# Kernel tuning notes

Measured on AMD Instinct MI355X. Metric: run time of the kernel, lower is better.

Reference implementation:

```python
import jax, jax.numpy as jnp
import numpy as np

TEMPERATURE = 0.1
KNN = 5
NEG = -1e30   # finite stand-in for -inf: identical softmax/threshold result, NaN-safe
EPS = -1e-08  # note: the original code really adds a NEGATIVE epsilon
MASK_VAL = -1.0


def setup_inputs() -> dict:
    key = jax.random.key(0)
    k1, k2, k3, k4 = jax.random.split(key, 4)
    n_img, max_r, n_cap, max_w, d = 128, 36, 128, 32, 512
    imgs = jax.random.normal(k1, (n_img, max_r, d), dtype=jnp.float32)
    caps = jax.random.normal(k2, (n_cap, max_w, d), dtype=jnp.float32)
    img_lens = jax.random.randint(k3, (n_img,), KNN + 1, max_r + 1, dtype=jnp.int32)
    cap_lens = jax.random.randint(k4, (n_cap,), 4, max_w + 1, dtype=jnp.int32)
    # guarantee lens.max() equals the static dims (torch slices to lens.max())
    img_lens = img_lens.at[0].set(max_r)
    cap_lens = cap_lens.at[0].set(max_w)
    return {"imgs": imgs, "caps": caps, "img_lens": img_lens, "cap_lens": cap_lens}


def reference(imgs, caps, img_lens, cap_lens):
    n_img, max_r, d = imgs.shape
    n_cap, max_w, _ = caps.shape
    knn = min(KNN, max_r)

    img_valid = jnp.arange(max_r)[None, :] < img_lens[:, None]   # [n_img, max_r]
    cap_valid = jnp.arange(max_w)[None, :] < cap_lens[:, None]   # [n_cap, max_w]
    imgs = jnp.where(img_valid[..., None], imgs, 0.0)
    caps = jnp.where(cap_valid[..., None], caps, 0.0)

    # fine-grained all-pairs similarities: [n_cap, n_img, max_w, max_r]
    sims = jnp.einsum('cwd,ird->ciwr', caps, imgs) / TEMPERATURE
    mask = cap_valid[:, None, :, None] & img_valid[None, :, None, :]
    sims = jnp.where(mask, sims, NEG)

    # top-KNN threshold along region axis (== sort()[..., max_r-KNN] in torch)
    kth = jax.lax.top_k(sims, knn)[0][..., -1:]
    sims = jnp.where(sims < kth, NEG, sims)

    attn = jax.nn.softmax(sims, axis=-1)
    attn = jnp.where(mask, attn, 0.0)

    att = jnp.einsum('ciwr,ird->ciwd', attn, imgs)                # attended regions
    num = jnp.einsum('ciwd,cwd->ciw', att, caps)
    den = jnp.linalg.norm(att, axis=-1) + EPS
    out = num / den                                               # [n_cap, n_img, max_w]
    out = jnp.where(cap_valid[:, None, :], out, MASK_VAL)
    return jnp.transpose(out, (1, 0, 2))                          # [n_img, n_cap, max_w]
```

## Files before the change

### kernel.cpp

```cpp
#include <hip/hip_runtime.h>
#include <cmath>

#define N_IMG 128
#define MAX_R 36
#define N_CAP 128
#define MAX_W 32
#define DIM   512
#define NEGV  -1e30f

typedef unsigned short u16;
typedef unsigned int   u32;
typedef unsigned char  u8;
typedef __attribute__((ext_vector_type(4))) int i32x4;

#define NI_ELEMS (N_IMG * MAX_R * DIM)
#define NC_ELEMS (N_CAP * MAX_W * DIM)

#define A_CHUNK 18432
#define B_CHUNK 16384
#define BUF_BYTES 34816
#define LDS_BYTES 69632

__device__ __forceinline__ void gload_lds16(const void* g, void* l) {
    __builtin_amdgcn_global_load_lds(
        (const __attribute__((address_space(1))) void*)g,
        (__attribute__((address_space(3))) void*)l, 16, 0, 0);
}

__global__ __launch_bounds__(256) void convert_kernel(const float* __restrict__ imgs,
                                                      const float* __restrict__ caps,
                                                      u8* __restrict__ imgsT,
                                                      u8* __restrict__ capsT) {
    const size_t ni4 = NI_ELEMS / 4;
    const size_t total4 = (NI_ELEMS + NC_ELEMS) / 4;
    const size_t stride = (size_t)gridDim.x * blockDim.x;
    for (size_t p = (size_t)blockIdx.x * blockDim.x + threadIdx.x; p < total4; p += stride) {
        const bool isImg = p < ni4;
        const float4 v = isImg ? ((const float4*)imgs)[p] : ((const float4*)caps)[p - ni4];
        const int q0 = (int)rintf(fminf(fmaxf(v.x * 4096.f, -32639.f), 32639.f));
        const int q1 = (int)rintf(fminf(fmaxf(v.y * 4096.f, -32639.f), 32639.f));
        const int q2 = (int)rintf(fminf(fmaxf(v.z * 4096.f, -32639.f), 32639.f));
        const int q3 = (int)rintf(fminf(fmaxf(v.w * 4096.f, -32639.f), 32639.f));
        const int h0 = (q0 + 128) >> 8, l0 = q0 - (h0 << 8);
        const int h1 = (q1 + 128) >> 8, l1 = q1 - (h1 << 8);
        const int h2 = (q2 + 128) >> 8, l2 = q2 - (h2 << 8);
        const int h3 = (q3 + 128) >> 8, l3 = q3 - (h3 << 8);
        const u32 hw = (u32)(h0 & 255) | ((u32)(h1 & 255) << 8) |
                       ((u32)(h2 & 255) << 16) | ((u32)(h3 & 255) << 24);
        const u32 lw = (u32)(l0 & 255) | ((u32)(l1 & 255) << 8) |
                       ((u32)(l2 & 255) << 16) | ((u32)(l3 & 255) << 24);
        if (isImg) {
            const int e = (int)(p * 4);
            const int imgRow = e >> 9, k = e & 511;
            const int g = imgRow / 144;
            const int rowT = imgRow - g * 144;
            const int kb = k >> 6, k6 = k & 63;
            const int blk = (k6 >> 4) ^ ((rowT >> 1) & 3);
            const size_t off = (size_t)(g * 8 + kb) * A_CHUNK + rowT * 64 + blk * 16 + (k6 & 15);
            *(u32*)(imgsT + off) = hw;
            *(u32*)(imgsT + off + 9216) = lw;
        } else {
            const int e = (int)((p - ni4) * 4);
            const int R = e >> 9, k = e & 511;
            const int cg = R >> 7, row = R & 127;
            const int kb = k >> 6, k6 = k & 63;
            const int blk = (k6 >> 4) ^ ((row >> 1) & 3);
            const size_t off = (size_t)(cg * 8 + kb) * B_CHUNK + row * 64 + blk * 16 + (k6 & 15);
            *(u32*)(capsT + off) = hw;
            *(u32*)(capsT + off + 8192) = lw;
        }
    }
}

__global__ __launch_bounds__(256) void gram_i8_kernel(const u8* __restrict__ imgsT,
                                                      float* __restrict__ G) {
    const int i  = blockIdx.x;
    const int gg = i >> 2;
    const int m  = i & 3;
    const int t = threadIdx.x;
    const int wid = t >> 6;
    const int lane = t & 63;
    const int l15 = lane & 15;
    const int kq = lane >> 4;

    __shared__ __align__(16) u8 sT[2][2][3072];

    const u8* base = imgsT + (size_t)gg * 8 * A_CHUNK + m * 36 * 64;

    auto stage = [&](int kb, int buf) {
        const u8* hsrc = base + (size_t)kb * A_CHUNK;
        {
            const int u = t;
            if (u < 144) gload_lds16(hsrc + u * 16, &sT[buf][0][u * 16]);
            else if (u < 288) gload_lds16(hsrc + 9216 + (u - 144) * 16, &sT[buf][1][(u - 144) * 16]);
        }
        if (t < 32) {
            const int u = 112 + t;
            gload_lds16(hsrc + 9216 + u * 16, &sT[buf][1][u * 16]);
        }
    };

    i32x4 aH[3], aC[3], aL[3];
    #pragma unroll
    for (int mt = 0; mt < 3; ++mt) {
        aH[mt] = (i32x4){0,0,0,0};
        aC[mt] = (i32x4){0,0,0,0};
        aL[mt] = (i32x4){0,0,0,0};
    }

    stage(0, 0);
    __syncthreads();

    const int m18 = 18 * m;
    for (int kb = 0; kb < 8; ++kb) {
        const int buf = kb & 1;
        if (kb < 7) stage(kb + 1, buf ^ 1);
        if (wid < 3) {
            const int brow = wid * 16 + l15;
            const int bblk = kq ^ ((m18 + (brow >> 1)) & 3);
            const i32x4 bh = *(const i32x4*)&sT[buf][0][brow * 64 + bblk * 16];
            const i32x4 bl = *(const i32x4*)&sT[buf][1][brow * 64 + bblk * 16];
            #pragma unroll
            for (int mt = 0; mt < 3; ++mt) {
                const int arow = mt * 16 + l15;
                const int ablk = kq ^ ((m18 + (arow >> 1)) & 3);
                const i32x4 ah = *(const i32x4*)&sT[buf][0][arow * 64 + ablk * 16];
                const i32x4 al = *(const i32x4*)&sT[buf][1][arow * 64 + ablk * 16];
                aH[mt] = __builtin_amdgcn_mfma_i32_16x16x64_i8(ah, bh, aH[mt], 0, 0, 0);
                aC[mt] = __builtin_amdgcn_mfma_i32_16x16x64_i8(ah, bl, aC[mt], 0, 0, 0);
                aC[mt] = __builtin_amdgcn_mfma_i32_16x16x64_i8(al, bh, aC[mt], 0, 0, 0);
                aL[mt] = __builtin_amdgcn_mfma_i32_16x16x64_i8(al, bl, aL[mt], 0, 0, 0);
            }
        }
        __syncthreads();
    }

    if (wid < 3) {
        const int col = wid * 16 + l15;
        if (col < 36) {
            #pragma unroll
            for (int mt = 0; mt < 3; ++mt) {
                #pragma unroll
                for (int e = 0; e < 4; ++e) {
                    const int row = mt * 16 + kq * 4 + e;
                    if (row < 36) {
                        const float g = (float)aH[mt][e] * (1.f / 256.f)
                                      + (float)aC[mt][e] * (1.f / 65536.f)
                                      + (float)aL[mt][e] * (1.f / 16777216.f);
                        G[(size_t)i * 1296 + row * 36 + col] = g;
                    }
                }
            }
        }
    }
}

__global__ __launch_bounds__(256, 2) void vsc_mfma_kernel(const u8* __restrict__ imgsT,
                                const u8* __restrict__ capsT,
                                const int* __restrict__ img_lens,
                                const int* __restrict__ cap_lens,
                                const float* __restrict__ G,
                                float* __restrict__ out) {
    extern __shared__ __align__(16) char smem[];
    const int bid = blockIdx.x;
    const int xcd = bid & 7;
    const int r_  = bid >> 3;
    const int g   = (r_ >> 5) * 8 + xcd;
    const int cg  = r_ & 31;
    const int t = threadIdx.x;
    const int wid = t >> 6;
    const int lane = t & 63;
    const int l15 = lane & 15;
    const int kblk = lane >> 4;

    const u8* gA = imgsT + (size_t)g * 8 * A_CHUNK;
    const u8* gB = capsT + (size_t)cg * 8 * B_CHUNK;

    auto stage = [&](int kb, char* buf) {
        if (wid < 2) {
            const u8* src = gA + (size_t)kb * A_CHUNK + wid * 9216 + lane * 16;
            char* dst = buf + wid * 9216;
            #pragma unroll
            for (int jj = 0; jj < 9; ++jj)
                gload_lds16(src + jj * 1024, dst + jj * 1024);
        } else {
            const int wb = wid - 2;
            const u8* src = gB + (size_t)kb * B_CHUNK + wb * 8192 + lane * 16;
            char* dst = buf + 18432 + wb * 8192;
            #pragma unroll
            for (int jj = 0; jj < 8; ++jj)
                gload_lds16(src + jj * 1024, dst + jj * 1024);
        }
    };

    i32x4 accH[9][2], accC[9][2];
    #pragma unroll
    for (int mt = 0; mt < 9; ++mt)
        #pragma unroll
        for (int nt = 0; nt < 2; ++nt) {
            accH[mt][nt] = (i32x4){0, 0, 0, 0};
            accC[mt][nt] = (i32x4){0, 0, 0, 0};
        }

    stage(0, smem);

    const int blk16 = (kblk ^ ((l15 >> 1) & 3)) << 4;
    const int baseA = l15 * 64 + blk16;
    const int baseB = (wid * 32 + l15) * 64 + blk16;

    for (int kb = 0; kb < 8; ++kb) {
        asm volatile("s_waitcnt vmcnt(0)" ::: "memory");
        __builtin_amdgcn_sched_barrier(0);
        __builtin_amdgcn_s_barrier();
        __builtin_amdgcn_sched_barrier(0);

        char* cur = smem + (size_t)(kb & 1) * BUF_BYTES;
        if (kb < 7) stage(kb + 1, smem + (size_t)((kb + 1) & 1) * BUF_BYTES);

        const i32x4 bh0 = *(const i32x4*)(cur + 18432 + baseB);
        const i32x4 bl0 = *(const i32x4*)(cur + 26624 + baseB);
        const i32x4 bh1 = *(const i32x4*)(cur + 18432 + baseB + 1024);
        const i32x4 bl1 = *(const i32x4*)(cur + 26624 + baseB + 1024);
        __builtin_amdgcn_s_setprio(1);
        #pragma unroll
        for (int mt = 0; mt < 9; ++mt) {
            const i32x4 ah = *(const i32x4*)(cur + baseA + mt * 1024);
            const i32x4 al = *(const i32x4*)(cur + 9216 + baseA + mt * 1024);
            i32x4 lt0 = (i32x4){0, 0, 0, 0};
            i32x4 lt1 = (i32x4){0, 0, 0, 0};
            lt0 = __builtin_amdgcn_mfma_i32_16x16x64_i8(al, bl0, lt0, 0, 0, 0);
            lt1 = __builtin_amdgcn_mfma_i32_16x16x64_i8(al, bl1, lt1, 0, 0, 0);
            accH[mt][0] = __builtin_amdgcn_mfma_i32_16x16x64_i8(ah, bh0, accH[mt][0], 0, 0, 0);
            accH[mt][1] = __builtin_amdgcn_mfma_i32_16x16x64_i8(ah, bh1, accH[mt][1], 0, 0, 0);
            accC[mt][0] = __builtin_amdgcn_mfma_i32_16x16x64_i8(ah, bl0, accC[mt][0], 0, 0, 0);
            accC[mt][0] = __builtin_amdgcn_mfma_i32_16x16x64_i8(al, bh0, accC[mt][0], 0, 0, 0);
            accC[mt][1] = __builtin_amdgcn_mfma_i32_16x16x64_i8(ah, bl1, accC[mt][1], 0, 0, 0);
            accC[mt][1] = __builtin_amdgcn_mfma_i32_16x16x64_i8(al, bh1, accC[mt][1], 0, 0, 0);
            #pragma unroll
            for (int e = 0; e < 4; ++e) {
                accC[mt][0][e] += lt0[e] >> 8;
                accC[mt][1][e] += lt1[e] >> 8;
            }
        }
        __builtin_amdgcn_s_setprio(0);
    }

    __syncthreads();

    float* sG = (float*)smem;
    {
        const float4* src = (const float4*)(G + (size_t)g * 4 * 1296);
        for (int idx = t; idx < 1296; idx += 256)
            ((float4*)sG)[idx] = src[idx];
    }
    __syncthreads();

    int ilen_[4];
    #pragma unroll
    for (int j = 0; j < 4; ++j) ilen_[j] = img_lens[g * 4 + j];

    #pragma unroll
    for (int nt = 0; nt < 2; ++nt) {
        const int col = wid * 32 + nt * 16 + l15;
        const int c = cg * 4 + (col >> 5);
        const int w = col & 31;
        const int clen = cap_lens[c];
        #pragma unroll
        for (int j = 0; j < 4; ++j) {
            const int mtb = (36 * j) >> 4;
            const int ilenj = ilen_[j];
            float tv0 = NEGV, tv1 = NEGV, tv2 = NEGV, tv3 = NEGV, tv4 = NEGV;
            #pragma unroll
            for (int dm = 0; dm < 3; ++dm) {
                #pragma unroll
                for (int e = 0; e < 4; ++e) {
                    const int mt = mtb + dm;
                    const int r = mt * 16 + kblk * 4 + e;
                    const int rr = r - 36 * j;
                    const float sval = (float)accH[mt][nt][e] * (10.f / 256.f)
                                     + (float)accC[mt][nt][e] * (10.f / 65536.f);
                    float v = NEGV;
                    if ((unsigned)rr < (unsigned)ilenj)
                        v = __uint_as_float((__float_as_uint(sval) & ~63u) | (u32)rr);
                    const bool c0 = v > tv0, c1 = v > tv1, c2 = v > tv2, c3 = v > tv3, c4 = v > tv4;
                    const float n4 = c4 ? (c3 ? tv3 : v) : tv4;
                    const float n3 = c3 ? (c2 ? tv2 : v) : tv3;
                    const float n2 = c2 ? (c1 ? tv1 : v) : tv2;
                    const float n1 = c1 ? (c0 ? tv0 : v) : tv1;
                    const float n0 = c0 ? v : tv0;
                    tv0 = n0; tv1 = n1; tv2 = n2; tv3 = n3; tv4 = n4;
                }
            }
            float ta[5] = {tv0, tv1, tv2, tv3, tv4};
            #pragma unroll
            for (int st = 0; st < 2; ++st) {
                const int dx = 16 << st;
                float tb[5];
                #pragma unroll
                for (int s = 0; s < 5; ++s) tb[s] = __shfl_xor(ta[s], dx);
                float na[5];
                #pragma unroll
                for (int k = 0; k < 5; ++k) {
                    float best = fmaxf(ta[k], tb[k]);
                    #pragma unroll
                    for (int i2 = 1; i2 <= k; ++i2)
                        best = fmaxf(best, fminf(ta[i2 - 1], tb[k - i2]));
                    na[k] = best;
                }
                #pragma unroll
                for (int s = 0; s < 5; ++s) ta[s] = na[s];
            }
            const float m = ta[0];
            const float p0 = 1.f;
            const float p1 = expf(ta[1] - m);
            const float p2 = expf(ta[2] - m);
            const float p3 = expf(ta[3] - m);
            const float p4 = expf(ta[4] - m);
            const float sum = p0 + p1 + p2 + p3 + p4;
            const float num = p0 * ta[0] + p1 * ta[1] + p2 * ta[2] + p3 * ta[3] + p4 * ta[4];
            const int r0 = __float_as_uint(ta[0]) & 63;
            const int r1 = __float_as_uint(ta[1]) & 63;
            const int r2 = __float_as_uint(ta[2]) & 63;
            const int r3 = __float_as_uint(ta[3]) & 63;
            const int r4 = __float_as_uint(ta[4]) & 63;
            const float* gj = sG + j * 1296;
            const float pa = (kblk == 0) ? p0 : (kblk == 1) ? p1 : (kblk == 2) ? p2 : p3;
            const int   ra = (kblk == 0) ? r0 : (kblk == 1) ? r1 : (kblk == 2) ? r2 : r3;
            const float* grow = gj + ra * 36;
            float part = pa * (p0 * grow[r0] + p1 * grow[r1] + p2 * grow[r2]
                             + p3 * grow[r3] + p4 * grow[r4]);
            if (kblk == 0) {
                const float* grow4 = gj + r4 * 36;
                part += p4 * (p0 * grow4[r0] + p1 * grow4[r1] + p2 * grow4[r2]
                            + p3 * grow4[r3] + p4 * grow4[r4]);
            }
            part += __shfl_xor(part, 16);
            part += __shfl_xor(part, 32);
            if (kblk == j) {
                float result = -1.f;
                if (w < clen) {
                    const float inv = 1.f / sum;
                    const float a_ = 0.1f * num * inv;
                    const float den = sqrtf(part) * inv + (-1e-8f);
                    result = a_ / den;
                }
                out[((size_t)(g * 4 + j) * N_CAP + c) * MAX_W + w] = result;
            }
        }
    }
}

extern "C" void kernel_launch(void* const* d_in, const int* in_sizes, int n_in,
                              void* d_out, int out_size, void* d_ws, size_t ws_size,
                              hipStream_t stream) {
    const float* imgs     = (const float*)d_in[0];
    const float* caps     = (const float*)d_in[1];
    const int*   img_lens = (const int*)d_in[2];
    const int*   cap_lens = (const int*)d_in[3];
    float* out = (float*)d_out;

    float* G  = (float*)d_ws;
    u8* imgsT = (u8*)d_ws + 663552;
    u8* capsT = imgsT + (size_t)32 * 8 * A_CHUNK;

    hipFuncSetAttribute((const void*)vsc_mfma_kernel,
                        hipFuncAttributeMaxDynamicSharedMemorySize, LDS_BYTES);

    convert_kernel<<<2048, 256, 0, stream>>>(imgs, caps, imgsT, capsT);
    gram_i8_kernel<<<N_IMG, 256, 0, stream>>>(imgsT, G);
    vsc_mfma_kernel<<<1024, 256, LDS_BYTES, stream>>>(imgsT, capsT, img_lens, cap_lens, G, out);
}
```

Before: 79.02 us.

## Single-buffer B tile to cut LDS and raise occupancy, use fast math intrinsics

The B (caption) tile in LDS is now single-buffered while A stays double-buffered. This cuts LDS per block from about 68KB to 52KB, and the launch bounds are raised to 3 blocks per CU. B fragments are read into registers before a second barrier, and only then is the next stage issued, so the single B buffer can be overwritten safely. The epilogue also swaps expf, division and sqrtf for the fast __expf, rcp and sqrt intrinsics. The cost is an extra barrier per k-step and a tighter register budget, which may cause spills with the large accumulator arrays.

```diff
diff --git a/kernel.cpp b/kernel.cpp
--- a/kernel.cpp
+++ b/kernel.cpp
@@ -18,8 +18,10 @@
 
 #define A_CHUNK 18432
 #define B_CHUNK 16384
-#define BUF_BYTES 34816
-#define LDS_BYTES 69632
+#define LDS_BYTES 53248
+#define A0_OFF 0
+#define A1_OFF 18432
+#define B_OFF  36864
 
 __device__ __forceinline__ void gload_lds16(const void* g, void* l) {
     __builtin_amdgcn_global_load_lds(
@@ -155,7 +157,7 @@
     }
 }
 
-__global__ __launch_bounds__(256, 2) void vsc_mfma_kernel(const u8* __restrict__ imgsT,
+__global__ __launch_bounds__(256, 3) void vsc_mfma_kernel(const u8* __restrict__ imgsT,
                                 const u8* __restrict__ capsT,
                                 const int* __restrict__ img_lens,
                                 const int* __restrict__ cap_lens,
@@ -176,17 +178,17 @@
     const u8* gA = imgsT + (size_t)g * 8 * A_CHUNK;
     const u8* gB = capsT + (size_t)cg * 8 * B_CHUNK;
 
-    auto stage = [&](int kb, char* buf) {
+    auto stage = [&](int kb, int abuf) {
         if (wid < 2) {
             const u8* src = gA + (size_t)kb * A_CHUNK + wid * 9216 + lane * 16;
-            char* dst = buf + wid * 9216;
+            char* dst = smem + abuf * A1_OFF + wid * 9216;
             #pragma unroll
             for (int jj = 0; jj < 9; ++jj)
                 gload_lds16(src + jj * 1024, dst + jj * 1024);
         } else {
             const int wb = wid - 2;
             const u8* src = gB + (size_t)kb * B_CHUNK + wb * 8192 + lane * 16;
-            char* dst = buf + 18432 + wb * 8192;
+            char* dst = smem + B_OFF + wb * 8192;
             #pragma unroll
             for (int jj = 0; jj < 8; ++jj)
                 gload_lds16(src + jj * 1024, dst + jj * 1024);
@@ -202,7 +204,7 @@
             accC[mt][nt] = (i32x4){0, 0, 0, 0};
         }
 
-    stage(0, smem);
+    stage(0, 0);
 
     const int blk16 = (kblk ^ ((l15 >> 1) & 3)) << 4;
     const int baseA = l15 * 64 + blk16;
@@ -214,18 +216,24 @@
         __builtin_amdgcn_s_barrier();
         __builtin_amdgcn_sched_barrier(0);
 
-        char* cur = smem + (size_t)(kb & 1) * BUF_BYTES;
-        if (kb < 7) stage(kb + 1, smem + (size_t)((kb + 1) & 1) * BUF_BYTES);
-
-        const i32x4 bh0 = *(const i32x4*)(cur + 18432 + baseB);
-        const i32x4 bl0 = *(const i32x4*)(cur + 26624 + baseB);
-        const i32x4 bh1 = *(const i32x4*)(cur + 18432 + baseB + 1024);
-        const i32x4 bl1 = *(const i32x4*)(cur + 26624 + baseB + 1024);
+        char* curA = smem + (size_t)(kb & 1) * A1_OFF;
+
+        const i32x4 bh0 = *(const i32x4*)(smem + B_OFF + baseB);
+        const i32x4 bl0 = *(const i32x4*)(smem + B_OFF + 8192 + baseB);
+        const i32x4 bh1 = *(const i32x4*)(smem + B_OFF + baseB + 1024);
+        const i32x4 bl1 = *(const i32x4*)(smem + B_OFF + 8192 + baseB + 1024);
+        asm volatile("s_waitcnt lgkmcnt(0)" ::: "memory");
+        __builtin_amdgcn_sched_barrier(0);
+        __builtin_amdgcn_s_barrier();
+        __builtin_amdgcn_sched_barrier(0);
+
+        if (kb < 7) stage(kb + 1, (kb + 1) & 1);
+
         __builtin_amdgcn_s_setprio(1);
         #pragma unroll
         for (int mt = 0; mt < 9; ++mt) {
-            const i32x4 ah = *(const i32x4*)(cur + baseA + mt * 1024);
-            const i32x4 al = *(const i32x4*)(cur + 9216 + baseA + mt * 1024);
+            const i32x4 ah = *(const i32x4*)(curA + baseA + mt * 1024);
+            const i32x4 al = *(const i32x4*)(curA + 9216 + baseA + mt * 1024);
             i32x4 lt0 = (i32x4){0, 0, 0, 0};
             i32x4 lt1 = (i32x4){0, 0, 0, 0};
             lt0 = __builtin_amdgcn_mfma_i32_16x16x64_i8(al, bl0, lt0, 0, 0, 0);
@@ -312,10 +320,10 @@
             }
             const float m = ta[0];
             const float p0 = 1.f;
-            const float p1 = expf(ta[1] - m);
-            const float p2 = expf(ta[2] - m);
-            const float p3 = expf(ta[3] - m);
-            const float p4 = expf(ta[4] - m);
+            const float p1 = __expf(ta[1] - m);
+            const float p2 = __expf(ta[2] - m);
+            const float p3 = __expf(ta[3] - m);
+            const float p4 = __expf(ta[4] - m);
             const float sum = p0 + p1 + p2 + p3 + p4;
             const float num = p0 * ta[0] + p1 * ta[1] + p2 * ta[2] + p3 * ta[3] + p4 * ta[4];
             const int r0 = __float_as_uint(ta[0]) & 63;
@@ -339,10 +347,10 @@
             if (kblk == j) {
                 float result = -1.f;
                 if (w < clen) {
-                    const float inv = 1.f / sum;
+                    const float inv = __builtin_amdgcn_rcpf(sum);
                     const float a_ = 0.1f * num * inv;
-                    const float den = sqrtf(part) * inv + (-1e-8f);
-                    result = a_ / den;
+                    const float den = __builtin_amdgcn_sqrtf(part) * inv + (-1e-8f);
+                    result = a_ * __builtin_amdgcn_rcpf(den);
                 }
                 out[((size_t)(g * 4 + j) * N_CAP + c) * MAX_W + w] = result;
             }
```

Result: slower. 168.9 us (+113.8%).
